# Kernel tuning notes

Hardware: AMD Instinct MI355X
Metric: run time of the kernel (lower is better)

The kernel has to match this reference:

```python
import jax, jax.numpy as jnp
import numpy as np

NUM_HEADS = 16
D_K = 64
BATCH_SIZE = 64
NUM_EDGES = 32768


def setup_inputs() -> dict:
    key = jax.random.key(0)
    k1, k2, k3, k4 = jax.random.split(key, 4)
    global_query = jax.random.normal(k1, (NUM_HEADS, BATCH_SIZE, D_K), dtype=jnp.float32)
    local_key = jax.random.normal(k2, (NUM_HEADS, NUM_EDGES, D_K), dtype=jnp.float32)
    local_value = jax.random.normal(k3, (NUM_HEADS, NUM_EDGES, D_K), dtype=jnp.float32)
    batch = jnp.sort(jax.random.randint(k4, (NUM_EDGES,), 0, BATCH_SIZE, dtype=jnp.int64))
    return {"global_query": global_query, "local_key": local_key,
            "local_value": local_value, "batch": batch}


def reference(global_query, local_key, local_value, batch):
    # global_query: [h, b, d]; local_key/value: [h, e, d]; batch: [e] segment ids
    num_heads, batch_size, d_k = global_query.shape
    # seg[b, e] = True iff edge e belongs to graph b
    seg = batch[None, :] == jnp.arange(batch_size, dtype=batch.dtype)[:, None]  # [b, e]
    # NOTE: original module does NOT scale by sqrt(d_k) despite its name
    scores = jnp.einsum('hbd,hed->hbe', global_query, local_key)  # [h, b, e]
    # per-segment softmax: out-of-segment entries get -inf -> exactly 0 weight,
    # matching the original which only softmaxes over edges with batch == i
    masked = jnp.where(seg[None, :, :], scores, -jnp.inf)
    attn = jax.nn.softmax(masked, axis=-1)  # [h, b, e]; zeros outside segment
    output = jnp.einsum('hbe,hed->hbd', attn, local_value)  # [h, b, d]
    return output, attn
```

## Files before the change

### kernel.cpp

```cpp
#include <hip/hip_runtime.h>
#include <math.h>

#define NH 16
#define NB 64
#define DK 64
#define NE 32768

typedef float vf4 __attribute__((ext_vector_type(4)));


__global__ void seg_bounds_kernel(const int* __restrict__ batch, int* __restrict__ bounds) {
    int e = blockIdx.x * 256 + threadIdx.x;
    if (e >= NE) return;
    int be = batch[e];
    if (e == 0) {
        for (int b = 0; b <= be; ++b) bounds[b] = 0;
    } else {
        int bp = batch[e - 1];
        for (int b = bp + 1; b <= be; ++b) bounds[b] = e;
    }
    if (e == NE - 1) {
        for (int b = be + 1; b <= NB; ++b) bounds[b] = NE;
    }
}

__global__ __launch_bounds__(512) void scores_kernel(
    const float* __restrict__ Q,
    const float* __restrict__ K,
    const int*   __restrict__ bounds,
    float* __restrict__ ksc_base,
    float* __restrict__ stash)
{
    const int b    = blockIdx.x;
    const int h    = blockIdx.y;
    const int tid  = threadIdx.x;
    const int wave = tid >> 6;
    const int lane = tid & 63;

    const int start = bounds[b];
    const int end   = bounds[b + 1];

    float* ksc = ksc_base + (size_t)h * NE;

    __shared__ float qs[DK];
    __shared__ float sm[8], sl[8];

    if (tid < DK) qs[tid] = Q[((size_t)h * NB + b) * DK + tid];
    __syncthreads();

    const float4* q4 = (const float4*)qs;
    float m = -INFINITY, l = 0.f;
    for (int e = start + tid; e < end; e += 512) {
        const float4* kr = (const float4*)(K + ((size_t)h * NE + e) * DK);
        float sx = 0.f, sy = 0.f, sz = 0.f, sw = 0.f;
        #pragma unroll
        for (int i = 0; i < DK / 4; ++i) {
            float4 kv = kr[i];
            float4 qv = q4[i];
            sx = fmaf(kv.x, qv.x, sx);
            sy = fmaf(kv.y, qv.y, sy);
            sz = fmaf(kv.z, qv.z, sz);
            sw = fmaf(kv.w, qv.w, sw);
        }
        float s = (sx + sy) + (sz + sw);
        ksc[e] = s;
        float nm = fmaxf(m, s);
        l = l * __expf(m - nm) + __expf(s - nm);
        m = nm;
    }

    #pragma unroll
    for (int off = 32; off; off >>= 1) {
        float om = __shfl_xor(m, off);
        float ol = __shfl_xor(l, off);
        float nm = fmaxf(m, om);
        float t1 = (l  > 0.f) ? l  * __expf(m  - nm) : 0.f;
        float t2 = (ol > 0.f) ? ol * __expf(om - nm) : 0.f;
        m = nm; l = t1 + t2;
    }
    if (lane == 0) { sm[wave] = m; sl[wave] = l; }
    __syncthreads();

    if (tid == 0) {
        float M = -INFINITY;
        #pragma unroll
        for (int w = 0; w < 8; ++w) M = fmaxf(M, sm[w]);
        float L = 0.f;
        #pragma unroll
        for (int w = 0; w < 8; ++w) L += (sl[w] > 0.f) ? sl[w] * __expf(sm[w] - M) : 0.f;
        const float inv = (L > 0.f) ? 1.f / L : 0.f;
        stash[((size_t)h * NB + b) * DK + 0] = M;
        stash[((size_t)h * NB + b) * DK + 1] = inv;
    }
}

__global__ __launch_bounds__(256) void attn_write_kernel(
    const int*   __restrict__ batch,
    const float* __restrict__ ksc_base,
    const float* __restrict__ stash,
    float* __restrict__ attn)
{
    const unsigned idx = blockIdx.x * 256u + threadIdx.x;
    const int e4 = idx & (NE / 4 - 1);
    const int bh = idx >> 13;
    const int b  = bh & (NB - 1);
    const int e0 = e4 << 2;

    const int4 bt = *(const int4*)(batch + e0);
    vf4 r = (vf4)(0.f);
    if (bt.x == b || bt.y == b || bt.z == b || bt.w == b) {
        const float M   = stash[(size_t)bh * DK + 0];
        const float inv = stash[(size_t)bh * DK + 1];
        const int h = bh >> 6;
        const float4 s = *(const float4*)(ksc_base + (size_t)h * NE + e0);
        if (bt.x == b) r.x = __expf(s.x - M) * inv;
        if (bt.y == b) r.y = __expf(s.y - M) * inv;
        if (bt.z == b) r.z = __expf(s.z - M) * inv;
        if (bt.w == b) r.w = __expf(s.w - M) * inv;
    }
    __builtin_nontemporal_store(r, (vf4*)attn + idx);
}

__global__ __launch_bounds__(512) void out_kernel(
    const float* __restrict__ V,
    const int*   __restrict__ bounds,
    const float* __restrict__ attn,
    float* __restrict__ out)
{
    const int b    = blockIdx.x;
    const int h    = blockIdx.y;
    const int tid  = threadIdx.x;
    const int wave = tid >> 6;
    const int lane = tid & 63;

    const int start = bounds[b];
    const int end   = bounds[b + 1];

    const float* arow = attn + ((size_t)h * NB + b) * NE;

    __shared__ float red[8][DK];

    const int S   = end - start;
    const int per = (S + 7) >> 3;
    const int cb  = start + wave * per;
    const int ce  = (cb + per < end) ? cb + per : end;

    float a0 = 0.f, a1 = 0.f, a2 = 0.f, a3 = 0.f;
    int e = cb;
    for (; e + 3 < ce; e += 4) {
        float p0 = arow[e];
        float p1 = arow[e + 1];
        float p2 = arow[e + 2];
        float p3 = arow[e + 3];
        const float* vb = V + ((size_t)h * NE + e) * DK + lane;
        a0 = fmaf(p0, vb[0 * DK], a0);
        a1 = fmaf(p1, vb[1 * DK], a1);
        a2 = fmaf(p2, vb[2 * DK], a2);
        a3 = fmaf(p3, vb[3 * DK], a3);
    }
    for (; e < ce; ++e) {
        float p = arow[e];
        a0 = fmaf(p, V[((size_t)h * NE + e) * DK + lane], a0);
    }
    red[wave][lane] = (a0 + a1) + (a2 + a3);
    __syncthreads();
    if (wave == 0) {
        float r = 0.f;
        #pragma unroll
        for (int w = 0; w < 8; ++w) r += red[w][lane];
        out[((size_t)h * NB + b) * DK + lane] = r;
    }
}

extern "C" void kernel_launch(void* const* d_in, const int* in_sizes, int n_in,
                              void* d_out, int out_size, void* d_ws, size_t ws_size,
                              hipStream_t stream) {
    const float* Q     = (const float*)d_in[0];
    const float* K     = (const float*)d_in[1];
    const float* V     = (const float*)d_in[2];
    const int*   batch = (const int*)d_in[3];

    float* out  = (float*)d_out;
    float* attn = out + (size_t)NH * NB * DK;

    int*   bounds = (int*)d_ws;
    float* ksc    = (float*)d_ws + 128;

    seg_bounds_kernel<<<NE / 256, 256, 0, stream>>>(batch, bounds);

    dim3 grid(NB, NH);
    scores_kernel<<<grid, 512, 0, stream>>>(Q, K, bounds, ksc, out);

    const unsigned nvf4 = (unsigned)NH * NB * (NE / 4);
    attn_write_kernel<<<nvf4 / 256, 256, 0, stream>>>(batch, ksc, out, attn);

    out_kernel<<<grid, 512, 0, stream>>>(V, bounds, attn, out);
}
```

Before: 344.3 us.

## Fuse attn write and PV output into one kernel, split score work per segment

The scores kernel now splits each (head, segment) task into two halves across 2048 blocks. Each wave uses 16 lanes per edge, with coalesced float4 K loads and shuffle reductions, and each half writes its partial max and sum. The attn-write and output kernels are merged into one launch: 1024 blocks stream the dense attn matrix with a grid-stride loop, while the other 1024 blocks compute the output. The output blocks recompute probabilities from the stored scores instead of rereading attn, so they no longer depend on the attn write and the two jobs can overlap. In exchange the launch mixes heterogeneous block types and recomputes the exponentials.

```diff
diff --git a/kernel.cpp b/kernel.cpp
--- a/kernel.cpp
+++ b/kernel.cpp
@@ -24,53 +24,61 @@
     }
 }
 
-__global__ __launch_bounds__(512) void scores_kernel(
+__global__ __launch_bounds__(256) void scores_kernel(
     const float* __restrict__ Q,
     const float* __restrict__ K,
     const int*   __restrict__ bounds,
     float* __restrict__ ksc_base,
-    float* __restrict__ stash)
+    float* __restrict__ mstash)
 {
-    const int b    = blockIdx.x;
-    const int h    = blockIdx.y;
+    const int g    = blockIdx.x;
+    const int task = g >> 1;
+    const int half = g & 1;
+    const int h    = task >> 6;
+    const int b    = task & (NB - 1);
     const int tid  = threadIdx.x;
     const int wave = tid >> 6;
     const int lane = tid & 63;
+    const int j    = lane >> 4;
+    const int c    = lane & 15;
 
     const int start = bounds[b];
     const int end   = bounds[b + 1];
+    const int S     = end - start;
+    const int Sh    = (S + 1) >> 1;
+    const int s0    = start + half * Sh;
+    const int e1    = (s0 + Sh < end) ? s0 + Sh : end;
 
     float* ksc = ksc_base + (size_t)h * NE;
 
     __shared__ float qs[DK];
-    __shared__ float sm[8], sl[8];
-
+    __shared__ float sm[4], sl[4];
     if (tid < DK) qs[tid] = Q[((size_t)h * NB + b) * DK + tid];
     __syncthreads();
 
-    const float4* q4 = (const float4*)qs;
+    const float4 qc = ((const float4*)qs)[c];
+    const float4* K4 = (const float4*)(K + (size_t)h * NE * DK);
+
     float m = -INFINITY, l = 0.f;
-    for (int e = start + tid; e < end; e += 512) {
-        const float4* kr = (const float4*)(K + ((size_t)h * NE + e) * DK);
-        float sx = 0.f, sy = 0.f, sz = 0.f, sw = 0.f;
-        #pragma unroll
-        for (int i = 0; i < DK / 4; ++i) {
-            float4 kv = kr[i];
-            float4 qv = q4[i];
-            sx = fmaf(kv.x, qv.x, sx);
-            sy = fmaf(kv.y, qv.y, sy);
-            sz = fmaf(kv.z, qv.z, sz);
-            sw = fmaf(kv.w, qv.w, sw);
-        }
-        float s = (sx + sy) + (sz + sw);
-        ksc[e] = s;
-        float nm = fmaxf(m, s);
-        l = l * __expf(m - nm) + __expf(s - nm);
-        m = nm;
+    for (int e = s0 + wave * 4; e < e1; e += 16) {
+        const int  ej    = e + j;
+        const bool valid = ej < e1;
+        const int  el    = valid ? ej : e1 - 1;
+        const float4 kv = K4[(size_t)el * (DK / 4) + c];
+        float s = fmaf(kv.x, qc.x, fmaf(kv.y, qc.y, fmaf(kv.z, qc.z, kv.w * qc.w)));
+        #pragma unroll
+        for (int off = 1; off < 16; off <<= 1)
+            s += __shfl_xor(s, off);
+        if (valid) {
+            if (c == 0) ksc[ej] = s;
+            float nm = fmaxf(m, s);
+            l = l * __expf(m - nm) + __expf(s - nm);
+            m = nm;
+        }
     }
 
     #pragma unroll
-    for (int off = 32; off; off >>= 1) {
+    for (int off = 16; off < 64; off <<= 1) {
         float om = __shfl_xor(m, off);
         float ol = __shfl_xor(l, off);
         float nm = fmaxf(m, om);
@@ -84,91 +92,109 @@
     if (tid == 0) {
         float M = -INFINITY;
         #pragma unroll
-        for (int w = 0; w < 8; ++w) M = fmaxf(M, sm[w]);
+        for (int w = 0; w < 4; ++w) M = fmaxf(M, sm[w]);
         float L = 0.f;
         #pragma unroll
-        for (int w = 0; w < 8; ++w) L += (sl[w] > 0.f) ? sl[w] * __expf(sm[w] - M) : 0.f;
-        const float inv = (L > 0.f) ? 1.f / L : 0.f;
-        stash[((size_t)h * NB + b) * DK + 0] = M;
-        stash[((size_t)h * NB + b) * DK + 1] = inv;
-    }
-}
-
-__global__ __launch_bounds__(256) void attn_write_kernel(
+        for (int w = 0; w < 4; ++w) L += (sl[w] > 0.f) ? sl[w] * __expf(sm[w] - M) : 0.f;
+        mstash[(task * 2 + half) * 2 + 0] = M;
+        mstash[(task * 2 + half) * 2 + 1] = L;
+    }
+}
+
+__global__ __launch_bounds__(256) void bc_kernel(
     const int*   __restrict__ batch,
     const float* __restrict__ ksc_base,
-    const float* __restrict__ stash,
-    float* __restrict__ attn)
-{
-    const unsigned idx = blockIdx.x * 256u + threadIdx.x;
-    const int e4 = idx & (NE / 4 - 1);
-    const int bh = idx >> 13;
-    const int b  = bh & (NB - 1);
-    const int e0 = e4 << 2;
-
-    const int4 bt = *(const int4*)(batch + e0);
-    vf4 r = (vf4)(0.f);
-    if (bt.x == b || bt.y == b || bt.z == b || bt.w == b) {
-        const float M   = stash[(size_t)bh * DK + 0];
-        const float inv = stash[(size_t)bh * DK + 1];
-        const int h = bh >> 6;
-        const float4 s = *(const float4*)(ksc_base + (size_t)h * NE + e0);
-        if (bt.x == b) r.x = __expf(s.x - M) * inv;
-        if (bt.y == b) r.y = __expf(s.y - M) * inv;
-        if (bt.z == b) r.z = __expf(s.z - M) * inv;
-        if (bt.w == b) r.w = __expf(s.w - M) * inv;
-    }
-    __builtin_nontemporal_store(r, (vf4*)attn + idx);
-}
-
-__global__ __launch_bounds__(512) void out_kernel(
+    const float* __restrict__ mstash,
     const float* __restrict__ V,
     const int*   __restrict__ bounds,
-    const float* __restrict__ attn,
+    float* __restrict__ attn,
     float* __restrict__ out)
 {
-    const int b    = blockIdx.x;
-    const int h    = blockIdx.y;
-    const int tid  = threadIdx.x;
-    const int wave = tid >> 6;
-    const int lane = tid & 63;
-
-    const int start = bounds[b];
-    const int end   = bounds[b + 1];
-
-    const float* arow = attn + ((size_t)h * NB + b) * NE;
-
-    __shared__ float red[8][DK];
-
-    const int S   = end - start;
-    const int per = (S + 7) >> 3;
-    const int cb  = start + wave * per;
-    const int ce  = (cb + per < end) ? cb + per : end;
-
-    float a0 = 0.f, a1 = 0.f, a2 = 0.f, a3 = 0.f;
-    int e = cb;
-    for (; e + 3 < ce; e += 4) {
-        float p0 = arow[e];
-        float p1 = arow[e + 1];
-        float p2 = arow[e + 2];
-        float p3 = arow[e + 3];
-        const float* vb = V + ((size_t)h * NE + e) * DK + lane;
-        a0 = fmaf(p0, vb[0 * DK], a0);
-        a1 = fmaf(p1, vb[1 * DK], a1);
-        a2 = fmaf(p2, vb[2 * DK], a2);
-        a3 = fmaf(p3, vb[3 * DK], a3);
-    }
-    for (; e < ce; ++e) {
-        float p = arow[e];
-        a0 = fmaf(p, V[((size_t)h * NE + e) * DK + lane], a0);
-    }
-    red[wave][lane] = (a0 + a1) + (a2 + a3);
-    __syncthreads();
-    if (wave == 0) {
-        float r = 0.f;
-        #pragma unroll
-        for (int w = 0; w < 8; ++w) r += red[w][lane];
-        out[((size_t)h * NB + b) * DK + lane] = r;
+    const int blk = blockIdx.x;
+    const int tid = threadIdx.x;
+    __shared__ float red[4][16][4];
+
+    if (blk < 1024) {
+        const unsigned total = (unsigned)NH * NB * (NE / 4);
+        for (unsigned idx = blk * 256u + tid; idx < total; idx += 1024u * 256u) {
+            const int e4 = idx & (NE / 4 - 1);
+            const int bh = idx >> 13;
+            const int b  = bh & (NB - 1);
+            const int e0 = e4 << 2;
+            const int4 bt = *(const int4*)(batch + e0);
+            vf4 r = (vf4)(0.f);
+            if (bt.x == b || bt.y == b || bt.z == b || bt.w == b) {
+                const float m0 = mstash[bh * 4 + 0], l0 = mstash[bh * 4 + 1];
+                const float m1 = mstash[bh * 4 + 2], l1 = mstash[bh * 4 + 3];
+                const float M = fmaxf(m0, m1);
+                float L = 0.f;
+                if (l0 > 0.f) L += l0 * __expf(m0 - M);
+                if (l1 > 0.f) L += l1 * __expf(m1 - M);
+                const float inv = (L > 0.f) ? 1.f / L : 0.f;
+                const int h = bh >> 6;
+                const float4 s = *(const float4*)(ksc_base + (size_t)h * NE + e0);
+                if (bt.x == b) r.x = __expf(s.x - M) * inv;
+                if (bt.y == b) r.y = __expf(s.y - M) * inv;
+                if (bt.z == b) r.z = __expf(s.z - M) * inv;
+                if (bt.w == b) r.w = __expf(s.w - M) * inv;
+            }
+            __builtin_nontemporal_store(r, (vf4*)attn + idx);
+        }
+    } else {
+        const int task = blk - 1024;
+        const int h    = task >> 6;
+        const int b    = task & (NB - 1);
+        const int wave = tid >> 6;
+        const int lane = tid & 63;
+        const int j    = lane >> 4;
+        const int c    = lane & 15;
+
+        const int start = bounds[b];
+        const int end   = bounds[b + 1];
+
+        const float m0 = mstash[task * 4 + 0], l0 = mstash[task * 4 + 1];
+        const float m1 = mstash[task * 4 + 2], l1 = mstash[task * 4 + 3];
+        const float M = fmaxf(m0, m1);
+        float L = 0.f;
+        if (l0 > 0.f) L += l0 * __expf(m0 - M);
+        if (l1 > 0.f) L += l1 * __expf(m1 - M);
+        const float inv = (L > 0.f) ? 1.f / L : 0.f;
+
+        const float*  ksc = ksc_base + (size_t)h * NE;
+        const float4* V4  = (const float4*)(V + (size_t)h * NE * DK);
+
+        float4 acc = make_float4(0.f, 0.f, 0.f, 0.f);
+        for (int e = start + wave * 4; e < end; e += 16) {
+            const int  ej    = e + j;
+            const bool valid = ej < end;
+            const int  el    = valid ? ej : end - 1;
+            const float p = valid ? __expf(ksc[ej] - M) * inv : 0.f;
+            const float4 v = V4[(size_t)el * (DK / 4) + c];
+            acc.x = fmaf(p, v.x, acc.x);
+            acc.y = fmaf(p, v.y, acc.y);
+            acc.z = fmaf(p, v.z, acc.z);
+            acc.w = fmaf(p, v.w, acc.w);
+        }
+        #pragma unroll
+        for (int off = 16; off < 64; off <<= 1) {
+            acc.x += __shfl_xor(acc.x, off);
+            acc.y += __shfl_xor(acc.y, off);
+            acc.z += __shfl_xor(acc.z, off);
+            acc.w += __shfl_xor(acc.w, off);
+        }
+        if (lane < 16) {
+            red[wave][c][0] = acc.x;
+            red[wave][c][1] = acc.y;
+            red[wave][c][2] = acc.z;
+            red[wave][c][3] = acc.w;
+        }
+        __syncthreads();
+        if (tid < DK) {
+            const int cc = tid >> 2, comp = tid & 3;
+            float r = red[0][cc][comp] + red[1][cc][comp]
+                    + red[2][cc][comp] + red[3][cc][comp];
+            out[((size_t)h * NB + b) * DK + tid] = r;
+        }
     }
 }
 
@@ -185,14 +211,11 @@
 
     int*   bounds = (int*)d_ws;
     float* ksc    = (float*)d_ws + 128;
+    float* mstash = ksc + (size_t)NH * NE;
 
     seg_bounds_kernel<<<NE / 256, 256, 0, stream>>>(batch, bounds);
 
-    dim3 grid(NB, NH);
-    scores_kernel<<<grid, 512, 0, stream>>>(Q, K, bounds, ksc, out);
-
-    const unsigned nvf4 = (unsigned)NH * NB * (NE / 4);
-    attn_write_kernel<<<nvf4 / 256, 256, 0, stream>>>(batch, ksc, out, attn);
-
-    out_kernel<<<grid, 512, 0, stream>>>(V, bounds, attn, out);
-}
+    scores_kernel<<<2048, 256, 0, stream>>>(Q, K, bounds, ksc, mstash);
+
+    bc_kernel<<<2048, 256, 0, stream>>>(batch, ksc, mstash, V, bounds, attn, out);
+}
```

After: 343.4 us. No clear change (-0.2%).
